# Optimization experiments

Measured on AMD Instinct MI355X. Metric: run time of the kernel, lower is better.

## Reference

```python
import jax, jax.numpy as jnp
import numpy as np

D_MODEL = 1024
NUM_HEADS = 16
HEAD_DIM = D_MODEL // NUM_HEADS
B, S = 2, 2048


def setup_inputs() -> dict:
    key = jax.random.key(0)
    ks = jax.random.split(key, 12)
    sc = 1.0 / np.sqrt(D_MODEL)
    return {
        "x": jax.random.normal(ks[0], (B, S, D_MODEL), dtype=jnp.float32),
        "Wq": jax.random.normal(ks[1], (D_MODEL, D_MODEL), dtype=jnp.float32) * sc,
        "bq": jnp.zeros((D_MODEL,), dtype=jnp.float32),
        "Wk": jax.random.normal(ks[2], (D_MODEL, D_MODEL), dtype=jnp.float32) * sc,
        "bk": jnp.zeros((D_MODEL,), dtype=jnp.float32),
        "Wv": jax.random.normal(ks[3], (D_MODEL, D_MODEL), dtype=jnp.float32) * sc,
        "bv": jnp.zeros((D_MODEL,), dtype=jnp.float32),
        "Wo": jax.random.normal(ks[4], (D_MODEL, D_MODEL), dtype=jnp.float32) * sc,
        "bo": jnp.zeros((D_MODEL,), dtype=jnp.float32),
        "gate": jax.random.normal(ks[5], (NUM_HEADS, HEAD_DIM), dtype=jnp.float32),
        "ent": jax.random.normal(ks[6], (NUM_HEADS, HEAD_DIM, HEAD_DIM), dtype=jnp.float32)
            * (1.0 / np.sqrt(HEAD_DIM)),
    }


def reference(x, Wq, bq, Wk, bk, Wv, bv, Wo, bo, gate, ent):
    b, s, _ = x.shape
    # QKV projections (torch Linear: x @ W^T + b)
    q = (x @ Wq.T + bq).reshape(b, s, NUM_HEADS, HEAD_DIM).transpose(0, 2, 1, 3)  # bhsd
    k = (x @ Wk.T + bk).reshape(b, s, NUM_HEADS, HEAD_DIM).transpose(0, 2, 1, 3)
    v = (x @ Wv.T + bv).reshape(b, s, NUM_HEADS, HEAD_DIM).transpose(0, 2, 1, 3)
    # superposition gate: per-head, per-dim sigmoid gate broadcast over sequence
    q = q * jax.nn.sigmoid(gate)[None, :, None, :]
    # entanglement: per-head small matmul on keys
    k = jnp.einsum("bhsd,hde->bhse", k, ent)
    scores = jnp.einsum("bhqd,bhkd->bhqk", q, k) / np.sqrt(HEAD_DIM)
    attn = jax.nn.softmax(scores, axis=-1)
    ctx = jnp.einsum("bhqk,bhkd->bhqd", attn, v)
    ctx = ctx.transpose(0, 2, 1, 3).reshape(b, s, D_MODEL)
    out = ctx @ Wo.T + bo
    return (out, attn)
```

## Files before the change

kernel.cpp:

```cpp
#include <hip/hip_runtime.h>
#include <hip/hip_bf16.h>

#define DM 1024
#define NH 16
#define HD 64
#define BATCH 2
#define SEQ 2048
#define MROWS (BATCH*SEQ)

typedef __attribute__((ext_vector_type(8))) short bf16x8;
typedef __attribute__((ext_vector_type(4))) short bf16x4;
typedef __attribute__((ext_vector_type(4))) float f32x4;
typedef __attribute__((ext_vector_type(4))) unsigned u32x4;

#define LOG2E 1.44269504088896f

__device__ __forceinline__ short f2b(float f) {
  union { float f; unsigned u; } x; x.f = f;
  unsigned r = x.u + 0x7fffu + ((x.u >> 16) & 1u);
  return (short)(r >> 16);
}

__device__ __forceinline__ unsigned cvtpk(float lo, float hi) {
  unsigned r;
  asm("v_cvt_pk_bf16_f32 %0, %1, %2" : "=v"(r) : "v"(lo), "v"(hi));
  return r;
}

__device__ __forceinline__ float nexp2(float x) {
  return __builtin_amdgcn_exp2f(x);
}

__device__ __forceinline__ void lds_barrier() {
  asm volatile("s_waitcnt lgkmcnt(0)" ::: "memory");
  __builtin_amdgcn_s_barrier();
}

__device__ __forceinline__ void gload16(const void* g, void* l) {
  __builtin_amdgcn_global_load_lds((const __attribute__((address_space(1))) unsigned int*)g,
                                   (__attribute__((address_space(3))) unsigned int*)l, 16, 0, 0);
}


__global__ void k_conv(const float* __restrict__ src, short* __restrict__ dst, int n) {
  int i = (blockIdx.x * 256 + threadIdx.x) * 8;
  if (i >= n) return;
  const float4* s4 = (const float4*)(src + i);
  float4 a = s4[0], b = s4[1];
  bf16x8 o;
  o[0]=f2b(a.x); o[1]=f2b(a.y); o[2]=f2b(a.z); o[3]=f2b(a.w);
  o[4]=f2b(b.x); o[5]=f2b(b.y); o[6]=f2b(b.z); o[7]=f2b(b.w);
  *(bf16x8*)(dst + i) = o;
}

__global__ void k_conv_gate(const float* __restrict__ Wq, const float* __restrict__ gate,
                            short* __restrict__ dst) {
  int i = (blockIdx.x * 256 + threadIdx.x) * 8;
  int row = i >> 10;
  float sg = (0.125f * LOG2E) / (1.f + __expf(-gate[row]));
  const float4* s4 = (const float4*)(Wq + i);
  float4 a = s4[0], b = s4[1];
  bf16x8 o;
  o[0]=f2b(a.x*sg); o[1]=f2b(a.y*sg); o[2]=f2b(a.z*sg); o[3]=f2b(a.w*sg);
  o[4]=f2b(b.x*sg); o[5]=f2b(b.y*sg); o[6]=f2b(b.z*sg); o[7]=f2b(b.w*sg);
  *(bf16x8*)(dst + i) = o;
}

__global__ void k_went(const float* __restrict__ Wk, const float* __restrict__ ent,
                       short* __restrict__ dst) {
  int r = blockIdx.x;
  int h = r >> 6, e = r & 63;
  int c = blockIdx.y * 256 + threadIdx.x;
  float acc = 0.f;
#pragma unroll 8
  for (int d = 0; d < 64; ++d)
    acc += ent[h*4096 + d*64 + e] * Wk[(size_t)(h*64 + d)*DM + c];
  dst[(size_t)r*DM + c] = f2b(acc);
}

__global__ void k_bias(const float* __restrict__ bq, const float* __restrict__ bk,
                       const float* __restrict__ bv, const float* __restrict__ gate,
                       const float* __restrict__ ent, float* __restrict__ bcat) {
  int i = blockIdx.x * 256 + threadIdx.x;
  float v;
  if (i < 1024) {
    v = bq[i] * ((0.125f * LOG2E) / (1.f + __expf(-gate[i])));
  } else if (i < 2048) {
    int rr = i - 1024, h = rr >> 6, e = rr & 63;
    float a = 0.f;
    for (int d = 0; d < 64; ++d) a += bk[h*64 + d] * ent[h*4096 + d*64 + e];
    v = a;
  } else {
    v = bv[i - 2048];
  }
  bcat[i] = v;
}


template<int MODE, int LGX>
__global__ __launch_bounds__(256) void gemm_bt(const short* __restrict__ A,
                                               const short* __restrict__ B,
                                               const float* __restrict__ bias,
                                               void* __restrict__ C,
                                               short* __restrict__ vt,
                                               int M, int N, int K) {
  __shared__ __align__(16) short As[128*64];
  __shared__ __align__(16) short Bs[128*64];
  const int t = threadIdx.x, l = t & 63, w = t >> 6;
  const int wr = w >> 1, wc = w & 1;
  const int lin = blockIdx.x + (blockIdx.y << LGX);
  const int nwg = gridDim.x * gridDim.y;
  const int virt = (lin & 7) * (nwg >> 3) + (lin >> 3);
  const int bm = virt & ((1 << LGX) - 1), bn = virt >> LGX;
  const int row_l = l & 15, kg = l >> 4;
  f32x4 acc[4][4];
  {
    f32x4 z = {0.f, 0.f, 0.f, 0.f};
#pragma unroll
    for (int m = 0; m < 4; ++m)
#pragma unroll
      for (int n = 0; n < 4; ++n) acc[m][n] = z;
  }
  for (int k0 = 0; k0 < K; k0 += 64) {
#pragma unroll
    for (int i = 0; i < 4; ++i) {
      int idx = i * 256 + t;
      int row = idx >> 3, cb = (idx & 7) * 8;
      gload16(A + (size_t)(bm*128 + row)*K + k0 + cb, &As[idx*8]);
      gload16(B + (size_t)(bn*128 + row)*K + k0 + cb, &Bs[idx*8]);
    }
    __syncthreads();
#pragma unroll
    for (int ks = 0; ks < 2; ++ks) {
      bf16x8 af[4], bfv[4];
#pragma unroll
      for (int m = 0; m < 4; ++m)
        af[m] = *(const bf16x8*)&As[(wr*64 + m*16 + row_l)*64 + ks*32 + kg*8];
#pragma unroll
      for (int n = 0; n < 4; ++n)
        bfv[n] = *(const bf16x8*)&Bs[(wc*64 + n*16 + row_l)*64 + ks*32 + kg*8];
#pragma unroll
      for (int m = 0; m < 4; ++m)
#pragma unroll
        for (int n = 0; n < 4; ++n)
          acc[m][n] = __builtin_amdgcn_mfma_f32_16x16x32_bf16(af[m], bfv[n], acc[m][n], 0, 0, 0);
    }
    __syncthreads();
  }
  const int r0 = bm*128 + wr*64, c0 = bn*128 + wc*64;
  if (MODE == 1 && c0 >= 2048) {
    const int bb = (bm*128) >> 11;
#pragma unroll
    for (int n = 0; n < 4; ++n) {
      int cv = c0 + n*16 + row_l - 2048;
      int hh = cv >> 6, dd = cv & 63;
      float bvs = bias[c0 + n*16 + row_l];
      short* vrow = vt + ((size_t)((bb*16 + hh)*64 + dd))*SEQ;
#pragma unroll
      for (int m = 0; m < 4; ++m) {
        int s0 = (r0 + m*16 + kg*4) & (SEQ-1);
        bf16x4 o;
        o[0]=f2b(acc[m][n][0]+bvs); o[1]=f2b(acc[m][n][1]+bvs);
        o[2]=f2b(acc[m][n][2]+bvs); o[3]=f2b(acc[m][n][3]+bvs);
        *(bf16x4*)&vrow[s0] = o;
      }
    }
  } else {
#pragma unroll
    for (int n = 0; n < 4; ++n) {
      int col = c0 + n*16 + row_l;
      float bvs = bias[col];
#pragma unroll
      for (int m = 0; m < 4; ++m) {
#pragma unroll
        for (int r = 0; r < 4; ++r) {
          int row = r0 + m*16 + kg*4 + r;
          float v = acc[m][n][r] + bvs;
          if (MODE == 1) ((short*)C)[(size_t)row*2048 + col] = f2b(v);
          else           ((float*)C)[(size_t)row*N + col] = v;
        }
      }
    }
  }
}

__global__ __launch_bounds__(256) void gemm_bt_small(const short* __restrict__ A,
                                                     const short* __restrict__ B,
                                                     const float* __restrict__ bias,
                                                     float* __restrict__ C,
                                                     int M, int N, int K) {
  __shared__ __align__(16) short As[64*64];
  __shared__ __align__(16) short Bs[128*64];
  const int t = threadIdx.x, l = t & 63, w = t >> 6;
  const int wr = w >> 1, wc = w & 1;
  const int lin = blockIdx.x + (blockIdx.y << 6);
  const int nwg = gridDim.x * gridDim.y;
  const int virt = (lin & 7) * (nwg >> 3) + (lin >> 3);
  const int bm = virt & 63, bn = virt >> 6;
  const int row_l = l & 15, kg = l >> 4;
  f32x4 acc[2][4];
  {
    f32x4 z = {0.f, 0.f, 0.f, 0.f};
#pragma unroll
    for (int m = 0; m < 2; ++m)
#pragma unroll
      for (int n = 0; n < 4; ++n) acc[m][n] = z;
  }
  for (int k0 = 0; k0 < K; k0 += 64) {
#pragma unroll
    for (int i = 0; i < 2; ++i) {
      int idx = i * 256 + t;
      int row = idx >> 3, cb = (idx & 7) * 8;
      gload16(A + (size_t)(bm*64 + row)*K + k0 + cb, &As[idx*8]);
    }
#pragma unroll
    for (int i = 0; i < 4; ++i) {
      int idx = i * 256 + t;
      int row = idx >> 3, cb = (idx & 7) * 8;
      gload16(B + (size_t)(bn*128 + row)*K + k0 + cb, &Bs[idx*8]);
    }
    __syncthreads();
#pragma unroll
    for (int ks = 0; ks < 2; ++ks) {
      bf16x8 af[2], bfv[4];
#pragma unroll
      for (int m = 0; m < 2; ++m)
        af[m] = *(const bf16x8*)&As[(wr*32 + m*16 + row_l)*64 + ks*32 + kg*8];
#pragma unroll
      for (int n = 0; n < 4; ++n)
        bfv[n] = *(const bf16x8*)&Bs[(wc*64 + n*16 + row_l)*64 + ks*32 + kg*8];
#pragma unroll
      for (int m = 0; m < 2; ++m)
#pragma unroll
        for (int n = 0; n < 4; ++n)
          acc[m][n] = __builtin_amdgcn_mfma_f32_16x16x32_bf16(af[m], bfv[n], acc[m][n], 0, 0, 0);
    }
    __syncthreads();
  }
  const int r0 = bm*64 + wr*32, c0 = bn*128 + wc*64;
#pragma unroll
  for (int n = 0; n < 4; ++n) {
    int col = c0 + n*16 + row_l;
    float bvs = bias[col];
#pragma unroll
    for (int m = 0; m < 2; ++m) {
#pragma unroll
      for (int r = 0; r < 4; ++r) {
        int row = r0 + m*16 + kg*4 + r;
        C[(size_t)row*N + col] = acc[m][n][r] + bvs;
      }
    }
  }
}


__global__ __launch_bounds__(256) void attn_fused(const short* __restrict__ qk,
                                                  const short* __restrict__ vtg,
                                                  float* __restrict__ attn_out,
                                                  short* __restrict__ ctx) {
  __shared__ __align__(16) short Ks[2][64*64];
  __shared__ __align__(16) short Vt[2][64*64];
  const int t = threadIdx.x, l = t & 63, w = t >> 6;
  const int row_l = l & 15, kg = l >> 4;
  const int rsl = row_l & 7;
  const int blk = blockIdx.x;
  const int bh = blk >> 5, q0 = (blk & 31) * 64;
  const int b = bh >> 4, h = bh & 15;
  const short* Qp = qk + (size_t)b*SEQ*2048 + h*64;
  const short* Kp = qk + (size_t)b*SEQ*2048 + 1024 + h*64;
  const short* Vg = vtg + (size_t)bh*64*SEQ;
  float* attn_bh = attn_out + (size_t)bh*SEQ*SEQ;
  const int qw = q0 + w*16;

  const bf16x8 aq0 = *(const bf16x8*)(Qp + (size_t)(qw + row_l)*2048 + kg*8);
  const bf16x8 aq1 = *(const bf16x8*)(Qp + (size_t)(qw + row_l)*2048 + 32 + kg*8);

  const int a0 = t >> 3, a1 = a0 + 32;
  const int c8 = (t & 7) * 8;
  const int g0 = (a0 & 0x23) | ((a0 & 0x0C) << 1) | ((a0 & 0x10) >> 2);
  const int g1 = (a1 & 0x23) | ((a1 & 0x0C) << 1) | ((a1 & 0x10) >> 2);
  const int wof0 = a0*64 + (c8 ^ ((a0 & 7) << 3));
  const int wof1 = a1*64 + (c8 ^ ((a0 & 7) << 3));

  float rsum = 0.f;
  {
    bf16x8 rk0 = *(const bf16x8*)(Kp + (size_t)g0*2048 + c8);
    bf16x8 rk1 = *(const bf16x8*)(Kp + (size_t)g1*2048 + c8);
    *(bf16x8*)&Ks[0][wof0] = rk0;
    *(bf16x8*)&Ks[0][wof1] = rk1;
  }
  lds_barrier();
#pragma unroll 1
  for (int kt = 0; kt < 32; ++kt) {
    const int cur = kt & 1;
    bf16x8 rk0, rk1;
    if (kt < 31) {
      const short* kb = Kp + (size_t)(kt + 1)*64*2048;
      rk0 = *(const bf16x8*)(kb + (size_t)g0*2048 + c8);
      rk1 = *(const bf16x8*)(kb + (size_t)g1*2048 + c8);
    }
    __builtin_amdgcn_s_setprio(1);
#pragma unroll
    for (int nt = 0; nt < 4; ++nt) {
      const int row = nt*16 + row_l;
      bf16x8 k0 = *(const bf16x8*)&Ks[cur][row*64 + ((kg ^ rsl) << 3)];
      bf16x8 k1 = *(const bf16x8*)&Ks[cur][row*64 + (((kg|4) ^ rsl) << 3)];
      f32x4 s = {0.f, 0.f, 0.f, 0.f};
      s = __builtin_amdgcn_mfma_f32_16x16x32_bf16(k0, aq0, s, 0, 0, 0);
      s = __builtin_amdgcn_mfma_f32_16x16x32_bf16(k1, aq1, s, 0, 0, 0);
      rsum += (nexp2(s[0]) + nexp2(s[1])) + (nexp2(s[2]) + nexp2(s[3]));
    }
    __builtin_amdgcn_s_setprio(0);
    if (kt < 31) {
      *(bf16x8*)&Ks[cur^1][wof0] = rk0;
      *(bf16x8*)&Ks[cur^1][wof1] = rk1;
    }
    lds_barrier();
  }
  rsum += __shfl_xor(rsum, 16);
  rsum += __shfl_xor(rsum, 32);
  const float inv = 1.f / rsum;

  f32x4 actx[4];
  {
    f32x4 z = {0.f, 0.f, 0.f, 0.f};
#pragma unroll
    for (int e = 0; e < 4; ++e) actx[e] = z;
  }

  {
    bf16x8 rk0 = *(const bf16x8*)(Kp + (size_t)g0*2048 + c8);
    bf16x8 rk1 = *(const bf16x8*)(Kp + (size_t)g1*2048 + c8);
    bf16x8 rv0 = *(const bf16x8*)(Vg + (size_t)a0*SEQ + c8);
    bf16x8 rv1 = *(const bf16x8*)(Vg + (size_t)a1*SEQ + c8);
    *(bf16x8*)&Ks[0][wof0] = rk0;
    *(bf16x8*)&Ks[0][wof1] = rk1;
    *(bf16x8*)&Vt[0][wof0] = rv0;
    *(bf16x8*)&Vt[0][wof1] = rv1;
  }
  lds_barrier();
#pragma unroll 1
  for (int kt = 0; kt < 32; ++kt) {
    const int cur = kt & 1;
    bf16x8 rk0, rk1, rv0, rv1;
    if (kt < 31) {
      const short* kb = Kp + (size_t)(kt + 1)*64*2048;
      const short* vb = Vg + (kt + 1)*64;
      rk0 = *(const bf16x8*)(kb + (size_t)g0*2048 + c8);
      rk1 = *(const bf16x8*)(kb + (size_t)g1*2048 + c8);
      rv0 = *(const bf16x8*)(vb + (size_t)a0*SEQ + c8);
      rv1 = *(const bf16x8*)(vb + (size_t)a1*SEQ + c8);
    }
    f32x4 pf[4];
    __builtin_amdgcn_s_setprio(1);
#pragma unroll
    for (int nt = 0; nt < 4; ++nt) {
      const int row = nt*16 + row_l;
      bf16x8 k0 = *(const bf16x8*)&Ks[cur][row*64 + ((kg ^ rsl) << 3)];
      bf16x8 k1 = *(const bf16x8*)&Ks[cur][row*64 + (((kg|4) ^ rsl) << 3)];
      f32x4 s = {0.f, 0.f, 0.f, 0.f};
      s = __builtin_amdgcn_mfma_f32_16x16x32_bf16(k0, aq0, s, 0, 0, 0);
      s = __builtin_amdgcn_mfma_f32_16x16x32_bf16(k1, aq1, s, 0, 0, 0);
      f32x4 p;
      p[0] = nexp2(s[0]) * inv; p[1] = nexp2(s[1]) * inv;
      p[2] = nexp2(s[2]) * inv; p[3] = nexp2(s[3]) * inv;
      *(f32x4*)&attn_bh[(size_t)(qw + row_l)*SEQ + kt*64 + (nt&2)*16 + kg*8 + (nt&1)*4] = p;
      pf[nt] = p;
    }
#pragma unroll
    for (int hh = 0; hh < 2; ++hh) {
      u32x4 pq;
      pq[0] = cvtpk(pf[2*hh][0],   pf[2*hh][1]);
      pq[1] = cvtpk(pf[2*hh][2],   pf[2*hh][3]);
      pq[2] = cvtpk(pf[2*hh+1][0], pf[2*hh+1][1]);
      pq[3] = cvtpk(pf[2*hh+1][2], pf[2*hh+1][3]);
      bf16x8 pb = *(bf16x8*)&pq;
      const int vslot = ((kg | (hh << 2)) ^ rsl) << 3;
#pragma unroll
      for (int e = 0; e < 4; ++e) {
        bf16x8 va = *(const bf16x8*)&Vt[cur][(e*16 + row_l)*64 + vslot];
        actx[e] = __builtin_amdgcn_mfma_f32_16x16x32_bf16(va, pb, actx[e], 0, 0, 0);
      }
    }
    __builtin_amdgcn_s_setprio(0);
    if (kt < 31) {
      *(bf16x8*)&Ks[cur^1][wof0] = rk0;
      *(bf16x8*)&Ks[cur^1][wof1] = rk1;
      *(bf16x8*)&Vt[cur^1][wof0] = rv0;
      *(bf16x8*)&Vt[cur^1][wof1] = rv1;
    }
    lds_barrier();
  }
#pragma unroll
  for (int e = 0; e < 4; ++e) {
    int2 o;
    o.x = (int)cvtpk(actx[e][0], actx[e][1]);
    o.y = (int)cvtpk(actx[e][2], actx[e][3]);
    *(int2*)&ctx[(size_t)(b*SEQ + qw + row_l)*DM + h*64 + e*16 + kg*4] = o;
  }
}


extern "C" void kernel_launch(void* const* d_in, const int* in_sizes, int n_in,
                              void* d_out, int out_size, void* d_ws, size_t ws_size,
                              hipStream_t stream) {
  const float* x    = (const float*)d_in[0];
  const float* Wq   = (const float*)d_in[1];
  const float* bq   = (const float*)d_in[2];
  const float* Wk   = (const float*)d_in[3];
  const float* bk   = (const float*)d_in[4];
  const float* Wv   = (const float*)d_in[5];
  const float* bv   = (const float*)d_in[6];
  const float* Wo   = (const float*)d_in[7];
  const float* bo   = (const float*)d_in[8];
  const float* gate = (const float*)d_in[9];
  const float* ent  = (const float*)d_in[10];

  char* ws = (char*)d_ws;
  short* xb   = (short*)(ws);
  short* Wcat = (short*)(ws + ((size_t)8  << 20));
  short* Wob  = (short*)(ws + ((size_t)14 << 20));
  float* bcat = (float*)(ws + ((size_t)16 << 20));
  short* qkb  = (short*)(ws + ((size_t)17 << 20));
  short* vtg  = (short*)(ws + ((size_t)33 << 20));
  short* ctxb = xb;

  float* outp  = (float*)d_out;
  float* attnp = outp + (size_t)MROWS * DM;

  k_conv<<<2048, 256, 0, stream>>>(x, xb, MROWS*DM);
  k_conv_gate<<<512, 256, 0, stream>>>(Wq, gate, Wcat);
  k_went<<<dim3(1024, 4), 256, 0, stream>>>(Wk, ent, Wcat + (size_t)1024*DM);
  k_conv<<<512, 256, 0, stream>>>(Wv, Wcat + (size_t)2048*DM, 1024*1024);
  k_conv<<<512, 256, 0, stream>>>(Wo, Wob, 1024*1024);
  k_bias<<<12, 256, 0, stream>>>(bq, bk, bv, gate, ent, bcat);

  gemm_bt<1, 5><<<dim3(32, 24), 256, 0, stream>>>(xb, Wcat, bcat, qkb, vtg, MROWS, 3072, DM);
  attn_fused<<<1024, 256, 0, stream>>>(qkb, vtg, attnp, ctxb);
  gemm_bt_small<<<dim3(64, 8), 256, 0, stream>>>(ctxb, Wob, bo, outp, MROWS, DM, DM);
}
```

Before: 285.5 us.

## Fuse prep kernels into one launch and widen attention blocks to 128 queries

Merges the six preprocessing kernels (x/weight conversions, gated Wq, entangled Wk, biases) into one k_prep launch, and rewrites the Wk·ent product to stage ent in LDS and accumulate 16 outputs per thread. The attention kernel moves to 512-thread blocks covering 128 query rows, so each K/V tile loaded into LDS is shared by twice as many waves and each thread loads one chunk instead of two. This cuts launch overhead and global K/V traffic, at the cost of fewer blocks (512) and heavier per-block synchronization.

After: 268.8 us. 1.06x faster.

```diff
diff --git a/kernel.cpp b/kernel.cpp
--- a/kernel.cpp
+++ b/kernel.cpp
@@ -41,59 +41,87 @@
                                    (__attribute__((address_space(3))) unsigned int*)l, 16, 0, 0);
 }
 
-
-__global__ void k_conv(const float* __restrict__ src, short* __restrict__ dst, int n) {
-  int i = (blockIdx.x * 256 + threadIdx.x) * 8;
-  if (i >= n) return;
-  const float4* s4 = (const float4*)(src + i);
-  float4 a = s4[0], b = s4[1];
-  bf16x8 o;
-  o[0]=f2b(a.x); o[1]=f2b(a.y); o[2]=f2b(a.z); o[3]=f2b(a.w);
-  o[4]=f2b(b.x); o[5]=f2b(b.y); o[6]=f2b(b.z); o[7]=f2b(b.w);
-  *(bf16x8*)(dst + i) = o;
-}
-
-__global__ void k_conv_gate(const float* __restrict__ Wq, const float* __restrict__ gate,
-                            short* __restrict__ dst) {
-  int i = (blockIdx.x * 256 + threadIdx.x) * 8;
-  int row = i >> 10;
-  float sg = (0.125f * LOG2E) / (1.f + __expf(-gate[row]));
-  const float4* s4 = (const float4*)(Wq + i);
-  float4 a = s4[0], b = s4[1];
-  bf16x8 o;
-  o[0]=f2b(a.x*sg); o[1]=f2b(a.y*sg); o[2]=f2b(a.z*sg); o[3]=f2b(a.w*sg);
-  o[4]=f2b(b.x*sg); o[5]=f2b(b.y*sg); o[6]=f2b(b.z*sg); o[7]=f2b(b.w*sg);
-  *(bf16x8*)(dst + i) = o;
-}
-
-__global__ void k_went(const float* __restrict__ Wk, const float* __restrict__ ent,
-                       short* __restrict__ dst) {
-  int r = blockIdx.x;
-  int h = r >> 6, e = r & 63;
-  int c = blockIdx.y * 256 + threadIdx.x;
-  float acc = 0.f;
-#pragma unroll 8
-  for (int d = 0; d < 64; ++d)
-    acc += ent[h*4096 + d*64 + e] * Wk[(size_t)(h*64 + d)*DM + c];
-  dst[(size_t)r*DM + c] = f2b(acc);
-}
-
-__global__ void k_bias(const float* __restrict__ bq, const float* __restrict__ bk,
-                       const float* __restrict__ bv, const float* __restrict__ gate,
-                       const float* __restrict__ ent, float* __restrict__ bcat) {
-  int i = blockIdx.x * 256 + threadIdx.x;
-  float v;
-  if (i < 1024) {
-    v = bq[i] * ((0.125f * LOG2E) / (1.f + __expf(-gate[i])));
-  } else if (i < 2048) {
-    int rr = i - 1024, h = rr >> 6, e = rr & 63;
-    float a = 0.f;
-    for (int d = 0; d < 64; ++d) a += bk[h*64 + d] * ent[h*4096 + d*64 + e];
-    v = a;
+__global__ __launch_bounds__(256) void k_prep(
+    const float* __restrict__ x,  const float* __restrict__ Wq,
+    const float* __restrict__ Wk, const float* __restrict__ Wv,
+    const float* __restrict__ Wo, const float* __restrict__ bq,
+    const float* __restrict__ bk, const float* __restrict__ bv,
+    const float* __restrict__ gate, const float* __restrict__ ent,
+    short* __restrict__ xb, short* __restrict__ Wcat,
+    short* __restrict__ Wob, float* __restrict__ bcat) {
+  __shared__ float entL[4096];
+  const int bid = blockIdx.x, t = threadIdx.x;
+  if (bid < 2048) {
+    int i = (bid * 256 + t) * 8;
+    const float4* s4 = (const float4*)(x + i);
+    float4 a = s4[0], b = s4[1];
+    bf16x8 o;
+    o[0]=f2b(a.x); o[1]=f2b(a.y); o[2]=f2b(a.z); o[3]=f2b(a.w);
+    o[4]=f2b(b.x); o[5]=f2b(b.y); o[6]=f2b(b.z); o[7]=f2b(b.w);
+    *(bf16x8*)(xb + i) = o;
+  } else if (bid < 2560) {
+    int i = ((bid - 2048) * 256 + t) * 8;
+    int row = i >> 10;
+    float sg = (0.125f * LOG2E) / (1.f + __expf(-gate[row]));
+    const float4* s4 = (const float4*)(Wq + i);
+    float4 a = s4[0], b = s4[1];
+    bf16x8 o;
+    o[0]=f2b(a.x*sg); o[1]=f2b(a.y*sg); o[2]=f2b(a.z*sg); o[3]=f2b(a.w*sg);
+    o[4]=f2b(b.x*sg); o[5]=f2b(b.y*sg); o[6]=f2b(b.z*sg); o[7]=f2b(b.w*sg);
+    *(bf16x8*)(Wcat + i) = o;
+  } else if (bid < 2624) {
+    int q = bid - 2560;
+    int h = q >> 2, cc = q & 3;
+    int c = cc * 256 + t;
+#pragma unroll
+    for (int j = 0; j < 16; ++j) entL[t + j*256] = ent[h*4096 + t + j*256];
+    __syncthreads();
+#pragma unroll 1
+    for (int ec = 0; ec < 4; ++ec) {
+      float acc[16];
+#pragma unroll
+      for (int e = 0; e < 16; ++e) acc[e] = 0.f;
+#pragma unroll 4
+      for (int d = 0; d < 64; ++d) {
+        float wk = Wk[(size_t)(h*64 + d)*DM + c];
+#pragma unroll
+        for (int e = 0; e < 16; ++e) acc[e] += entL[d*64 + ec*16 + e] * wk;
+      }
+#pragma unroll
+      for (int e = 0; e < 16; ++e)
+        Wcat[(size_t)(1024 + h*64 + ec*16 + e)*DM + c] = f2b(acc[e]);
+    }
+  } else if (bid < 3136) {
+    int i = ((bid - 2624) * 256 + t) * 8;
+    const float4* s4 = (const float4*)(Wv + i);
+    float4 a = s4[0], b = s4[1];
+    bf16x8 o;
+    o[0]=f2b(a.x); o[1]=f2b(a.y); o[2]=f2b(a.z); o[3]=f2b(a.w);
+    o[4]=f2b(b.x); o[5]=f2b(b.y); o[6]=f2b(b.z); o[7]=f2b(b.w);
+    *(bf16x8*)(Wcat + (size_t)2048*DM + i) = o;
+  } else if (bid < 3648) {
+    int i = ((bid - 3136) * 256 + t) * 8;
+    const float4* s4 = (const float4*)(Wo + i);
+    float4 a = s4[0], b = s4[1];
+    bf16x8 o;
+    o[0]=f2b(a.x); o[1]=f2b(a.y); o[2]=f2b(a.z); o[3]=f2b(a.w);
+    o[4]=f2b(b.x); o[5]=f2b(b.y); o[6]=f2b(b.z); o[7]=f2b(b.w);
+    *(bf16x8*)(Wob + i) = o;
   } else {
-    v = bv[i - 2048];
-  }
-  bcat[i] = v;
+    int i = (bid - 3648) * 256 + t;
+    float v;
+    if (i < 1024) {
+      v = bq[i] * ((0.125f * LOG2E) / (1.f + __expf(-gate[i])));
+    } else if (i < 2048) {
+      int rr = i - 1024, h = rr >> 6, e = rr & 63;
+      float a = 0.f;
+      for (int d = 0; d < 64; ++d) a += bk[h*64 + d] * ent[h*4096 + d*64 + e];
+      v = a;
+    } else {
+      v = bv[i - 2048];
+    }
+    bcat[i] = v;
+  }
 }
 
 
@@ -254,7 +282,7 @@
 }
 
 
-__global__ __launch_bounds__(256) void attn_fused(const short* __restrict__ qk,
+__global__ __launch_bounds__(512) void attn_fused(const short* __restrict__ qk,
                                                   const short* __restrict__ vtg,
                                                   float* __restrict__ attn_out,
                                                   short* __restrict__ ctx) {
@@ -264,7 +292,7 @@
   const int row_l = l & 15, kg = l >> 4;
   const int rsl = row_l & 7;
   const int blk = blockIdx.x;
-  const int bh = blk >> 5, q0 = (blk & 31) * 64;
+  const int bh = blk >> 4, q0 = (blk & 15) * 128;
   const int b = bh >> 4, h = bh & 15;
   const short* Qp = qk + (size_t)b*SEQ*2048 + h*64;
   const short* Kp = qk + (size_t)b*SEQ*2048 + 1024 + h*64;
@@ -275,29 +303,24 @@
   const bf16x8 aq0 = *(const bf16x8*)(Qp + (size_t)(qw + row_l)*2048 + kg*8);
   const bf16x8 aq1 = *(const bf16x8*)(Qp + (size_t)(qw + row_l)*2048 + 32 + kg*8);
 
-  const int a0 = t >> 3, a1 = a0 + 32;
+  const int a0 = t >> 3;
   const int c8 = (t & 7) * 8;
   const int g0 = (a0 & 0x23) | ((a0 & 0x0C) << 1) | ((a0 & 0x10) >> 2);
-  const int g1 = (a1 & 0x23) | ((a1 & 0x0C) << 1) | ((a1 & 0x10) >> 2);
   const int wof0 = a0*64 + (c8 ^ ((a0 & 7) << 3));
-  const int wof1 = a1*64 + (c8 ^ ((a0 & 7) << 3));
 
   float rsum = 0.f;
   {
     bf16x8 rk0 = *(const bf16x8*)(Kp + (size_t)g0*2048 + c8);
-    bf16x8 rk1 = *(const bf16x8*)(Kp + (size_t)g1*2048 + c8);
     *(bf16x8*)&Ks[0][wof0] = rk0;
-    *(bf16x8*)&Ks[0][wof1] = rk1;
   }
   lds_barrier();
 #pragma unroll 1
   for (int kt = 0; kt < 32; ++kt) {
     const int cur = kt & 1;
-    bf16x8 rk0, rk1;
+    bf16x8 rk0;
     if (kt < 31) {
       const short* kb = Kp + (size_t)(kt + 1)*64*2048;
       rk0 = *(const bf16x8*)(kb + (size_t)g0*2048 + c8);
-      rk1 = *(const bf16x8*)(kb + (size_t)g1*2048 + c8);
     }
     __builtin_amdgcn_s_setprio(1);
 #pragma unroll
@@ -313,7 +336,6 @@
     __builtin_amdgcn_s_setprio(0);
     if (kt < 31) {
       *(bf16x8*)&Ks[cur^1][wof0] = rk0;
-      *(bf16x8*)&Ks[cur^1][wof1] = rk1;
     }
     lds_barrier();
   }
@@ -330,26 +352,20 @@
 
   {
     bf16x8 rk0 = *(const bf16x8*)(Kp + (size_t)g0*2048 + c8);
-    bf16x8 rk1 = *(const bf16x8*)(Kp + (size_t)g1*2048 + c8);
     bf16x8 rv0 = *(const bf16x8*)(Vg + (size_t)a0*SEQ + c8);
-    bf16x8 rv1 = *(const bf16x8*)(Vg + (size_t)a1*SEQ + c8);
     *(bf16x8*)&Ks[0][wof0] = rk0;
-    *(bf16x8*)&Ks[0][wof1] = rk1;
     *(bf16x8*)&Vt[0][wof0] = rv0;
-    *(bf16x8*)&Vt[0][wof1] = rv1;
   }
   lds_barrier();
 #pragma unroll 1
   for (int kt = 0; kt < 32; ++kt) {
     const int cur = kt & 1;
-    bf16x8 rk0, rk1, rv0, rv1;
+    bf16x8 rk0, rv0;
     if (kt < 31) {
       const short* kb = Kp + (size_t)(kt + 1)*64*2048;
       const short* vb = Vg + (kt + 1)*64;
       rk0 = *(const bf16x8*)(kb + (size_t)g0*2048 + c8);
-      rk1 = *(const bf16x8*)(kb + (size_t)g1*2048 + c8);
       rv0 = *(const bf16x8*)(vb + (size_t)a0*SEQ + c8);
-      rv1 = *(const bf16x8*)(vb + (size_t)a1*SEQ + c8);
     }
     f32x4 pf[4];
     __builtin_amdgcn_s_setprio(1);
@@ -385,9 +401,7 @@
     __builtin_amdgcn_s_setprio(0);
     if (kt < 31) {
       *(bf16x8*)&Ks[cur^1][wof0] = rk0;
-      *(bf16x8*)&Ks[cur^1][wof1] = rk1;
       *(bf16x8*)&Vt[cur^1][wof0] = rv0;
-      *(bf16x8*)&Vt[cur^1][wof1] = rv1;
     }
     lds_barrier();
   }
@@ -428,14 +442,9 @@
   float* outp  = (float*)d_out;
   float* attnp = outp + (size_t)MROWS * DM;
 
-  k_conv<<<2048, 256, 0, stream>>>(x, xb, MROWS*DM);
-  k_conv_gate<<<512, 256, 0, stream>>>(Wq, gate, Wcat);
-  k_went<<<dim3(1024, 4), 256, 0, stream>>>(Wk, ent, Wcat + (size_t)1024*DM);
-  k_conv<<<512, 256, 0, stream>>>(Wv, Wcat + (size_t)2048*DM, 1024*1024);
-  k_conv<<<512, 256, 0, stream>>>(Wo, Wob, 1024*1024);
-  k_bias<<<12, 256, 0, stream>>>(bq, bk, bv, gate, ent, bcat);
-
+  k_prep<<<3660, 256, 0, stream>>>(x, Wq, Wk, Wv, Wo, bq, bk, bv, gate, ent,
+                                   xb, Wcat, Wob, bcat);
   gemm_bt<1, 5><<<dim3(32, 24), 256, 0, stream>>>(xb, Wcat, bcat, qkb, vtg, MROWS, 3072, DM);
-  attn_fused<<<1024, 256, 0, stream>>>(qkb, vtg, attnp, ctxb);
+  attn_fused<<<512, 512, 0, stream>>>(qkb, vtg, attnp, ctxb);
   gemm_bt_small<<<dim3(64, 8), 256, 0, stream>>>(ctxb, Wob, bo, outp, MROWS, DM, DM);
 }
```
